# Kernel tuning notes

Measured on AMD Instinct MI355X. Metric: run time of the kernel, lower is better.

The kernel has to match this reference:

```python
import jax, jax.numpy as jnp
import numpy as np

# init_kwargs baked in as module constants
N, K, CONV_DIM = 20, 10, 512
T, ALPHA = 0.1, 0.1
BNORM = 1.0  # self.B == 2 only when N==K==5
BATCH = 256


def setup_inputs() -> dict:
    key = jax.random.key(0)
    op = jax.random.normal(key, (BATCH, N, K, 1, CONV_DIM), dtype=jnp.float32)
    return {"op": op}


def reference(op):
    # op: [B, N, K, 1, D]
    p = jnp.squeeze(op, axis=-2)                                  # [B,N,K,D]
    p = p / jnp.linalg.norm(p, axis=-1, keepdims=True)            # L2 normalize
    b = p.shape[0]
    all_p = p.reshape(b, N * K, CONV_DIM)                         # [B,NK,D] (n-major, k-minor, same as split+concat)

    # vectorized over all N*K anchors: pairwise similarities to all prototypes
    sims = jnp.einsum('bnkd,bmd->bnkm', p, all_p) / T             # [B,N,K,NK]
    self_sim = jnp.sum(p * p, axis=-1) / T                        # [B,N,K] (== 1/T after normalization)

    # denominator: sum of exp over all prototypes minus the anchor itself
    exp_term = jnp.sum(jnp.exp(sims), axis=-1) - jnp.exp(self_sim)  # [B,N,K]
    log_term = jnp.log(exp_term)

    # positive term: mean similarity to same-class prototypes excluding anchor
    pos = jnp.einsum('bnkd,bnjd->bnk', p, p) / T                  # sum over class members incl. self
    sum_term = (pos - self_sim) / (K - 1)                         # [B,N,K]

    cl_loss = jnp.sum(log_term - sum_term)                        # sums over batch and all anchors
    return ALPHA * cl_loss / (BNORM * N * K * CONV_DIM)
```

## Files before the change

### kernel.cpp

```cpp
#include <hip/hip_runtime.h>
#include <hip/hip_bf16.h>
#include <math.h>

#define BATCH   256
#define KMEM    10
#define NPROT   200
#define DDIM    512
#define TINVF   10.0f
#define KSLAB   64
#define NSLAB   (DDIM / KSLAB)
#define RPAD    256
#define ROWB    128
#define NSEG    800

typedef __attribute__((ext_vector_type(8))) short short8;
typedef __attribute__((ext_vector_type(4))) float f32x4;

__device__ __forceinline__ unsigned short f2bf(float v) {
    unsigned u = __float_as_uint(v);
    return (unsigned short)((u + 0x7fffu + ((u >> 16) & 1u)) >> 16);
}

__device__ __forceinline__ void pack16(const float4 c[4], uint4& p0, uint4& p1, float& sq) {
    union { unsigned short us[16]; uint4 u[2]; } w;
    const float* f = (const float*)c;
    #pragma unroll
    for (int e = 0; e < 16; e++) {
        float v = f[e];
        sq = fmaf(v, v, sq);
        w.us[e] = f2bf(v);
    }
    p0 = w.u[0];
    p1 = w.u[1];
}

__global__ __launch_bounds__(512, 2) void kmain(const float* __restrict__ P,
                                                float* __restrict__ partial) {
    __shared__ char  slab[2][RPAD * ROWB];
    __shared__ float normpart[NSEG];
    __shared__ float invn_s[RPAD];
    __shared__ float s1buf[2][RPAD];
    __shared__ float s2buf[2][RPAD];
    __shared__ float red[512];

    const int tid  = threadIdx.x;
    const int lane = tid & 63;
    const int wave = tid >> 6;
    const int wr   = wave >> 1;
    const int wc   = wave & 1;
    const int b    = blockIdx.x;
    const float* Pb = P + (size_t)b * NPROT * DDIM;

    for (int z = tid; z < 2 * 56 * 8; z += 512) {
        int bsel = z / (56 * 8);
        int slot = z % (56 * 8);
        int row  = NPROT + (slot >> 3);
        *(uint4*)(&slab[bsel][row * ROWB + (slot & 7) * 16]) = make_uint4(0, 0, 0, 0);
    }

    const int  idx0 = tid;
    const int  row0 = idx0 >> 2, seg0 = idx0 & 3;
    const int  idx1 = tid + 512;
    const bool has1 = (idx1 < NSEG);
    const int  row1 = idx1 >> 2, seg1 = idx1 & 3;

    float sq0 = 0.f, sq1 = 0.f;

    float4 curA[4], curB[4];
    {
        const float4* sA = (const float4*)(Pb + (size_t)row0 * DDIM + seg0 * 16);
        curA[0] = sA[0]; curA[1] = sA[1]; curA[2] = sA[2]; curA[3] = sA[3];
        if (has1) {
            const float4* sB = (const float4*)(Pb + (size_t)row1 * DDIM + seg1 * 16);
            curB[0] = sB[0]; curB[1] = sB[1]; curB[2] = sB[2]; curB[3] = sB[3];
        }
    }

    f32x4 acc[4][8];
    #pragma unroll
    for (int i = 0; i < 4; i++)
        #pragma unroll
        for (int j = 0; j < 8; j++)
            acc[i][j] = (f32x4)(0.f);

    const int swz0 = (row0 & 7) << 4;
    const int swz1 = (row1 & 7) << 4;

    for (int s = 0; s < NSLAB; s++) {
        char* buf = slab[s & 1];

        {
            uint4 p0, p1;
            pack16(curA, p0, p1, sq0);
            int byte0 = row0 * ROWB + seg0 * 32;
            *(uint4*)(&buf[(byte0     ) ^ swz0]) = p0;
            *(uint4*)(&buf[(byte0 + 16) ^ swz0]) = p1;
        }
        if (has1) {
            uint4 p0, p1;
            pack16(curB, p0, p1, sq1);
            int byte0 = row1 * ROWB + seg1 * 32;
            *(uint4*)(&buf[(byte0     ) ^ swz1]) = p0;
            *(uint4*)(&buf[(byte0 + 16) ^ swz1]) = p1;
        }
        __syncthreads();

        float4 nxtA[4], nxtB[4];
        if (s + 1 < NSLAB) {
            const float4* sA = (const float4*)(Pb + (size_t)row0 * DDIM + (s + 1) * KSLAB + seg0 * 16);
            nxtA[0] = sA[0]; nxtA[1] = sA[1]; nxtA[2] = sA[2]; nxtA[3] = sA[3];
            if (has1) {
                const float4* sB = (const float4*)(Pb + (size_t)row1 * DDIM + (s + 1) * KSLAB + seg1 * 16);
                nxtB[0] = sB[0]; nxtB[1] = sB[1]; nxtB[2] = sB[2]; nxtB[3] = sB[3];
            }
        }

        #pragma unroll
        for (int ks = 0; ks < 2; ks++) {
            const int kb = (ks * 32 + (lane >> 4) * 8) * 2;
            short8 af[4];
            #pragma unroll
            for (int i = 0; i < 4; i++) {
                int row = (wr * 4 + i) * 16 + (lane & 15);
                af[i] = *(const short8*)(&buf[(row * ROWB + kb) ^ ((row & 7) << 4)]);
            }
            #pragma unroll
            for (int j = 0; j < 8; j++) {
                int row = (wc * 8 + j) * 16 + (lane & 15);
                short8 bf = *(const short8*)(&buf[(row * ROWB + kb) ^ ((row & 7) << 4)]);
                #pragma unroll
                for (int i = 0; i < 4; i++)
                    acc[i][j] = __builtin_amdgcn_mfma_f32_16x16x32_bf16(af[i], bf, acc[i][j], 0, 0, 0);
            }
        }

        #pragma unroll
        for (int q = 0; q < 4; q++) { curA[q] = nxtA[q]; curB[q] = nxtB[q]; }
    }

    normpart[idx0] = sq0;
    if (has1) normpart[idx1] = sq1;
    __syncthreads();
    if (tid < RPAD) {
        float iv = 0.f;
        if (tid < NPROT) {
            float ns = normpart[4 * tid] + normpart[4 * tid + 1]
                     + normpart[4 * tid + 2] + normpart[4 * tid + 3];
            iv = rsqrtf(ns);
        }
        invn_s[tid] = iv;
    }
    __syncthreads();

    float ijn[8]; int jg[8], jdiv[8];
    #pragma unroll
    for (int j = 0; j < 8; j++) {
        jg[j]   = wc * 128 + j * 16 + (lane & 15);
        ijn[j]  = invn_s[jg[j]];
        jdiv[j] = jg[j] / KMEM;
    }
    #pragma unroll
    for (int i = 0; i < 4; i++) {
        #pragma unroll
        for (int r = 0; r < 4; r++) {
            const int m = wr * 64 + i * 16 + (lane >> 4) * 4 + r;
            const float im = invn_s[m];
            const int mdiv = m / KMEM;
            float s1 = 0.f, s2 = 0.f;
            #pragma unroll
            for (int j = 0; j < 8; j++) {
                float g = acc[i][j][r] * im * ijn[j];
                bool valid = (jg[j] < NPROT) && (m < NPROT) && (jg[j] != m);
                s1 += valid ? __expf(g * TINVF) : 0.f;
                s2 += (valid && (jdiv[j] == mdiv)) ? g : 0.f;
            }
            #pragma unroll
            for (int d = 1; d < 16; d <<= 1) {
                s1 += __shfl_xor(s1, d);
                s2 += __shfl_xor(s2, d);
            }
            if ((lane & 15) == 0) {
                s1buf[wc][m] = s1;
                s2buf[wc][m] = s2;
            }
        }
    }
    __syncthreads();

    float v = 0.f;
    if (tid < NPROT) {
        float S1 = s1buf[0][tid] + s1buf[1][tid];
        float S2 = s2buf[0][tid] + s2buf[1][tid];
        v = logf(S1) - S2 * (TINVF / 9.0f);
    }
    red[tid] = v;
    __syncthreads();
    for (int sx = 256; sx > 0; sx >>= 1) {
        if (tid < sx) red[tid] += red[tid + sx];
        __syncthreads();
    }
    if (tid == 0) partial[b] = red[0];
}

__global__ __launch_bounds__(256) void kfinal(const float* __restrict__ partial,
                                              float* __restrict__ out) {
    __shared__ double red[256];
    int tid = threadIdx.x;
    red[tid] = (double)partial[tid];
    __syncthreads();
    for (int sx = 128; sx > 0; sx >>= 1) {
        if (tid < sx) red[tid] += red[tid + sx];
        __syncthreads();
    }
    if (tid == 0) out[0] = (float)(red[0] * (0.1 / 102400.0));
}

extern "C" void kernel_launch(void* const* d_in, const int* in_sizes, int n_in,
                              void* d_out, int out_size, void* d_ws, size_t ws_size,
                              hipStream_t stream) {
    const float* P = (const float*)d_in[0];
    float* partial = (float*)d_ws;
    float* out     = (float*)d_out;

    kmain<<<BATCH, 512, 0, stream>>>(P, partial);
    kfinal<<<1, 256, 0, stream>>>(partial, out);
}
```

Baseline: 33.72 us.

## Split each batch's Gram matrix columns across two blocks with post-reduction kernel

Each batch item is now handled by two blocks, each computing half of the 256 column tiles of the similarity matrix. This halves the accumulator registers per wave and doubles the grid from 256 to 512 blocks, so the 256 CUs of the device can be filled more fully. Partial row sums are written to workspace, and a new kpost kernel combines the two halves and applies the log term. The cost is that both blocks reload and convert the full input rows, doubling global reads and normalisation work, and an extra kernel launch is added.

```diff
diff --git a/kernel.cpp b/kernel.cpp
--- a/kernel.cpp
+++ b/kernel.cpp
@@ -12,6 +12,7 @@
 #define RPAD    256
 #define ROWB    128
 #define NSEG    800
+#define NBLK    (BATCH * 2)
 
 typedef __attribute__((ext_vector_type(8))) short short8;
 typedef __attribute__((ext_vector_type(4))) float f32x4;
@@ -34,21 +35,22 @@
     p1 = w.u[1];
 }
 
-__global__ __launch_bounds__(512, 2) void kmain(const float* __restrict__ P,
-                                                float* __restrict__ partial) {
+__global__ __launch_bounds__(512) void kmain(const float* __restrict__ P,
+                                             float* __restrict__ s12) {
     __shared__ char  slab[2][RPAD * ROWB];
     __shared__ float normpart[NSEG];
     __shared__ float invn_s[RPAD];
     __shared__ float s1buf[2][RPAD];
     __shared__ float s2buf[2][RPAD];
-    __shared__ float red[512];
 
     const int tid  = threadIdx.x;
     const int lane = tid & 63;
     const int wave = tid >> 6;
     const int wr   = wave >> 1;
     const int wc   = wave & 1;
-    const int b    = blockIdx.x;
+    const int hb   = blockIdx.x;
+    const int half = (hb >> 3) & 1;
+    const int b    = ((hb >> 4) << 3) | (hb & 7);
     const float* Pb = P + (size_t)b * NPROT * DDIM;
 
     for (int z = tid; z < 2 * 56 * 8; z += 512) {
@@ -63,6 +65,8 @@
     const int  idx1 = tid + 512;
     const bool has1 = (idx1 < NSEG);
     const int  row1 = idx1 >> 2, seg1 = idx1 & 3;
+    const int  swz0 = (row0 & 7) << 4;
+    const int  swz1 = (row1 & 7) << 4;
 
     float sq0 = 0.f, sq1 = 0.f;
 
@@ -76,15 +80,12 @@
         }
     }
 
-    f32x4 acc[4][8];
+    f32x4 acc[4][4];
     #pragma unroll
     for (int i = 0; i < 4; i++)
         #pragma unroll
-        for (int j = 0; j < 8; j++)
+        for (int j = 0; j < 4; j++)
             acc[i][j] = (f32x4)(0.f);
-
-    const int swz0 = (row0 & 7) << 4;
-    const int swz1 = (row1 & 7) << 4;
 
     for (int s = 0; s < NSLAB; s++) {
         char* buf = slab[s & 1];
@@ -125,12 +126,12 @@
                 af[i] = *(const short8*)(&buf[(row * ROWB + kb) ^ ((row & 7) << 4)]);
             }
             #pragma unroll
-            for (int j = 0; j < 8; j++) {
-                int row = (wc * 8 + j) * 16 + (lane & 15);
-                short8 bf = *(const short8*)(&buf[(row * ROWB + kb) ^ ((row & 7) << 4)]);
+            for (int j = 0; j < 4; j++) {
+                int row = (half * 8 + wc * 4 + j) * 16 + (lane & 15);
+                short8 bfr = *(const short8*)(&buf[(row * ROWB + kb) ^ ((row & 7) << 4)]);
                 #pragma unroll
                 for (int i = 0; i < 4; i++)
-                    acc[i][j] = __builtin_amdgcn_mfma_f32_16x16x32_bf16(af[i], bf, acc[i][j], 0, 0, 0);
+                    acc[i][j] = __builtin_amdgcn_mfma_f32_16x16x32_bf16(af[i], bfr, acc[i][j], 0, 0, 0);
             }
         }
 
@@ -152,10 +153,10 @@
     }
     __syncthreads();
 
-    float ijn[8]; int jg[8], jdiv[8];
-    #pragma unroll
-    for (int j = 0; j < 8; j++) {
-        jg[j]   = wc * 128 + j * 16 + (lane & 15);
+    float ijn[4]; int jg[4], jdiv[4];
+    #pragma unroll
+    for (int j = 0; j < 4; j++) {
+        jg[j]   = half * 128 + wc * 64 + j * 16 + (lane & 15);
         ijn[j]  = invn_s[jg[j]];
         jdiv[j] = jg[j] / KMEM;
     }
@@ -168,7 +169,7 @@
             const int mdiv = m / KMEM;
             float s1 = 0.f, s2 = 0.f;
             #pragma unroll
-            for (int j = 0; j < 8; j++) {
+            for (int j = 0; j < 4; j++) {
                 float g = acc[i][j][r] * im * ijn[j];
                 bool valid = (jg[j] < NPROT) && (m < NPROT) && (jg[j] != m);
                 s1 += valid ? __expf(g * TINVF) : 0.f;
@@ -187,26 +188,43 @@
     }
     __syncthreads();
 
+    if (tid < RPAD) {
+        float S1 = s1buf[0][tid] + s1buf[1][tid];
+        float S2 = s2buf[0][tid] + s2buf[1][tid];
+        s12[(size_t)hb * (2 * RPAD) + tid * 2    ] = S1;
+        s12[(size_t)hb * (2 * RPAD) + tid * 2 + 1] = S2;
+    }
+}
+
+__global__ __launch_bounds__(256) void kpost(const float* __restrict__ s12,
+                                             float* __restrict__ partial2) {
+    __shared__ float red[256];
+    const int b   = blockIdx.x;
+    const int tid = threadIdx.x;
+    const int hb0 = ((b >> 3) << 4) | (b & 7);
+    const int hb1 = hb0 | 8;
     float v = 0.f;
     if (tid < NPROT) {
-        float S1 = s1buf[0][tid] + s1buf[1][tid];
-        float S2 = s2buf[0][tid] + s2buf[1][tid];
+        float S1 = s12[(size_t)hb0 * (2 * RPAD) + tid * 2    ]
+                 + s12[(size_t)hb1 * (2 * RPAD) + tid * 2    ];
+        float S2 = s12[(size_t)hb0 * (2 * RPAD) + tid * 2 + 1]
+                 + s12[(size_t)hb1 * (2 * RPAD) + tid * 2 + 1];
         v = logf(S1) - S2 * (TINVF / 9.0f);
     }
     red[tid] = v;
     __syncthreads();
-    for (int sx = 256; sx > 0; sx >>= 1) {
+    for (int sx = 128; sx > 0; sx >>= 1) {
         if (tid < sx) red[tid] += red[tid + sx];
         __syncthreads();
     }
-    if (tid == 0) partial[b] = red[0];
-}
-
-__global__ __launch_bounds__(256) void kfinal(const float* __restrict__ partial,
+    if (tid == 0) partial2[b] = red[0];
+}
+
+__global__ __launch_bounds__(256) void kfinal(const float* __restrict__ partial2,
                                               float* __restrict__ out) {
     __shared__ double red[256];
     int tid = threadIdx.x;
-    red[tid] = (double)partial[tid];
+    red[tid] = (double)partial2[tid];
     __syncthreads();
     for (int sx = 128; sx > 0; sx >>= 1) {
         if (tid < sx) red[tid] += red[tid + sx];
@@ -218,10 +236,12 @@
 extern "C" void kernel_launch(void* const* d_in, const int* in_sizes, int n_in,
                               void* d_out, int out_size, void* d_ws, size_t ws_size,
                               hipStream_t stream) {
-    const float* P = (const float*)d_in[0];
-    float* partial = (float*)d_ws;
-    float* out     = (float*)d_out;
-
-    kmain<<<BATCH, 512, 0, stream>>>(P, partial);
-    kfinal<<<1, 256, 0, stream>>>(partial, out);
-}
+    const float* P  = (const float*)d_in[0];
+    float* s12      = (float*)d_ws;
+    float* partial2 = s12 + (size_t)NBLK * (2 * RPAD);
+    float* out      = (float*)d_out;
+
+    kmain<<<NBLK, 512, 0, stream>>>(P, s12);
+    kpost<<<BATCH, 256, 0, stream>>>(s12, partial2);
+    kfinal<<<1, 256, 0, stream>>>(partial2, out);
+}
```

Measured after the change: 45.57 us. +35.2%, slower.
